# Kernel optimization log

Measured on AMD Instinct MI355X. Metric: run time of the kernel, lower is better.

## Reference

```python
import jax, jax.numpy as jnp
import numpy as np

WIN = 12     # SAMv3 window_size
HEADS = 8    # num_heads

def _window(t, win=WIN):
    B, H, W, C = t.shape
    t = t.reshape(B, H // win, win, W // win, win, C).transpose(0, 1, 3, 2, 4, 5)
    return t.reshape(B, (H // win) * (W // win), win * win, C)

def _unwindow(t, H, W, win=WIN):
    B, nW, S, C = t.shape
    t = t.reshape(B, H // win, W // win, win, win, C).transpose(0, 1, 3, 2, 4, 5)
    return t.reshape(B, H, W, C)

def _sam(fq, fkv, bias, wq, wk, wv, wo, bo):
    # Windowed, masked cross-frame multi-head attention (SAMv3).
    # fq, fkv: (B, C, H, W); bias: (B, nW, 1, 1, S) additive mask bias.
    B, C, H, W = fq.shape
    hd = C // HEADS
    scale = hd ** -0.5
    q = _window(jnp.einsum('bchw,cd->bhwd', fq, wq))   # (B,nW,S,C)
    k = _window(jnp.einsum('bchw,cd->bhwd', fkv, wk))
    v = _window(jnp.einsum('bchw,cd->bhwd', fkv, wv))
    nW, S = q.shape[1], q.shape[2]
    q = q.reshape(B, nW, S, HEADS, hd)
    k = k.reshape(B, nW, S, HEADS, hd)
    v = v.reshape(B, nW, S, HEADS, hd)
    attn = jnp.einsum('bnqhd,bnkhd->bnhqk', q, k) * scale + bias
    attn = jax.nn.softmax(attn, axis=-1)
    out = jnp.einsum('bnhqk,bnkhd->bnqhd', attn, v).reshape(B, nW, S, C)
    out = out @ wo + bo
    return _unwindow(out, H, W).transpose(0, 3, 1, 2)  # (B, C, H, W)

def setup_inputs() -> dict:
    key = jax.random.key(0)
    B, C, T, H, W = 2, 384, 2, 192, 192
    ks = jax.random.split(key, 16)
    d = {}
    d['x'] = jax.random.normal(ks[0], (B, C, T, H, W), jnp.float32)
    d['mask'] = jax.random.randint(ks[1], (B, T, 1, H, W), 0, 2, jnp.int32)
    names = ['sam1_wq', 'sam1_wk', 'sam1_wv', 'sam1_wo',
             'sam2_wq', 'sam2_wk', 'sam2_wv', 'sam2_wo',
             'proj1_w', 'proj2_w']
    for i, n in enumerate(names):
        d[n] = jax.random.normal(ks[2 + i], (C, C), jnp.float32) * 0.02
    d['sam1_bo'] = jnp.zeros((C,), jnp.float32)
    d['sam2_bo'] = jnp.zeros((C,), jnp.float32)
    d['proj1_b'] = jnp.zeros((C,), jnp.float32)
    d['proj2_b'] = jnp.zeros((C,), jnp.float32)
    return d

def reference(x, mask, sam1_wq, sam1_wk, sam1_wv, sam1_wo, sam1_bo,
              sam2_wq, sam2_wk, sam2_wv, sam2_wo, sam2_bo,
              proj1_w, proj1_b, proj2_w, proj2_b):
    # x: (B, C, T=2, H, W); mask: (B, T, 1, H, W)
    f1 = x[:, :, 0]
    f2 = x[:, :, 1]
    m = mask[:, 1, 0][..., None]                      # (B, H, W, 1), frame-2 mask
    mw = _window(m)[..., 0]                           # (B, nW, S)
    bias = jnp.where(mw == 0, -1e9, 0.0).astype(x.dtype)[:, :, None, None, :]
    o1 = _sam(f1, f2, bias, sam1_wq, sam1_wk, sam1_wv, sam1_wo, sam1_bo)
    x1 = jnp.einsum('bchw,dc->bdhw', o1, proj1_w) + proj1_b[None, :, None, None]
    o2 = _sam(f2, f1, bias, sam2_wq, sam2_wk, sam2_wv, sam2_wo, sam2_bo)
    x2 = jnp.einsum('bchw,dc->bdhw', o2, proj2_w) + proj2_b[None, :, None, None]
    return jnp.concatenate([x1[:, :, None], x2[:, :, None]], axis=2)  # (B, C, 2, H, W)
```

## Files before the change

kernel.cpp:

```cpp
#include <hip/hip_runtime.h>
#include <stdint.h>

typedef __attribute__((ext_vector_type(8))) short bf16x8;
typedef __attribute__((ext_vector_type(4))) float f32x4;

#define HW    36864
#define CCH   384
#define NPIX  73728
#define W2    147456

__device__ __forceinline__ unsigned short f2bf(float f) {
  unsigned u = __builtin_bit_cast(unsigned, f);
  u += 0x7FFFu + ((u >> 16) & 1u);
  return (unsigned short)(u >> 16);
}

typedef const unsigned int __attribute__((address_space(1)))* gas1_t;
typedef unsigned int __attribute__((address_space(3)))* las3_t;
__device__ __forceinline__ void gload16(const void* g, void* l) {
  __builtin_amdgcn_global_load_lds((gas1_t)g, (las3_t)l, 16, 0, 0);
}


__global__ void k_wt(const float* __restrict__ w0, const float* __restrict__ w1,
                     const float* __restrict__ w2, const float* __restrict__ w3,
                     const float* __restrict__ w4, const float* __restrict__ w5,
                     unsigned short* __restrict__ wt) {
  int idx = blockIdx.x * 256 + threadIdx.x;
  int w = blockIdx.y;
  const float* W;
  switch (w) { case 0: W = w0; break; case 1: W = w1; break;
               case 2: W = w2; break; case 3: W = w3; break;
               case 4: W = w4; break; default: W = w5; break; }
  int c = idx / 384, d = idx % 384;
  wt[(size_t)w * W2 + (size_t)d * 384 + c] = f2bf(W[(size_t)c * 384 + d]);
}

__global__ void k_wf(const float* __restrict__ wo1, const float* __restrict__ pj1,
                     const float* __restrict__ wo2, const float* __restrict__ pj2,
                     unsigned short* __restrict__ wfT) {
  int idx = blockIdx.x * 256 + threadIdx.x;
  int s = blockIdx.y;
  const float* wo = s ? wo2 : wo1;
  const float* pj = s ? pj2 : pj1;
  int d = idx / 384, e = idx % 384;
  float acc = 0.f;
  for (int c = 0; c < 384; ++c) acc += pj[d * 384 + c] * wo[e * 384 + c];
  wfT[(size_t)s * W2 + (size_t)d * 384 + e] = f2bf(acc);
}

__global__ void k_bf(const float* __restrict__ bo1, const float* __restrict__ pj1,
                     const float* __restrict__ pb1, const float* __restrict__ bo2,
                     const float* __restrict__ pj2, const float* __restrict__ pb2,
                     float* __restrict__ bfused) {
  int t = threadIdx.x;
  int s = t / 384, d = t % 384;
  const float* bo = s ? bo2 : bo1;
  const float* pj = s ? pj2 : pj1;
  const float* pb = s ? pb2 : pb1;
  float acc = pb[d];
  for (int c = 0; c < 384; ++c) acc += pj[d * 384 + c] * bo[c];
  bfused[t] = acc;
}

__global__ __launch_bounds__(256) void k_tx(const float* __restrict__ x,
                                            unsigned short* __restrict__ xbf) {
  __shared__ float tile[64][65];
  int p0 = blockIdx.x * 64;
  int c0 = blockIdx.y * 64;
  int bt = blockIdx.z;
  int b = bt >> 1, t = bt & 1;
  int tid = threadIdx.x;
  int cl = tid >> 2;
  int pq = (tid & 3) * 4;
  const float* src = x + (((size_t)b * CCH + (c0 + cl)) * 2 + t) * HW + p0;
#pragma unroll
  for (int i = 0; i < 4; ++i) {
    int p_l = pq + i * 16;
    float4 v = *reinterpret_cast<const float4*>(src + p_l);
    tile[cl][p_l + 0] = v.x; tile[cl][p_l + 1] = v.y;
    tile[cl][p_l + 2] = v.z; tile[cl][p_l + 3] = v.w;
  }
  __syncthreads();
  int pl = tid >> 2;
  int cq = (tid & 3) * 16;
  unsigned short* dst = xbf + ((size_t)(t * 2 + b) * HW + p0 + pl) * CCH + c0 + cq;
  bf16x8 o0, o1;
#pragma unroll
  for (int j = 0; j < 8; ++j) o0[j] = (short)f2bf(tile[cq + j][pl]);
#pragma unroll
  for (int j = 0; j < 8; ++j) o1[j] = (short)f2bf(tile[cq + 8 + j][pl]);
  *reinterpret_cast<bf16x8*>(dst) = o0;
  *reinterpret_cast<bf16x8*>(dst + 8) = o1;
}

template <int EPI>
__global__ __launch_bounds__(256) void gemm_bt(
    const unsigned short* __restrict__ A,
    const unsigned short* __restrict__ Bt,
    unsigned short* __restrict__ Cb, int ldc,
    float* __restrict__ Cf,
    const float* __restrict__ bias,
    int tsel, float oscale) {
  __shared__ __align__(16) unsigned short Ash[2][4096];
  __shared__ __align__(16) unsigned short Bsh[2][4096];
  const int tid = threadIdx.x;
  const int lane = tid & 63;
  const int wid = tid >> 6, wr = wid >> 1, wc = wid & 1;
  const int m0 = blockIdx.y * 128, n0 = blockIdx.x * 128;
  const int r15 = lane & 15, g = lane >> 4;

  const int u1 = tid + 256;
  const unsigned short* srcA0 = A + (size_t)(m0 + (tid >> 2)) * 384 + (((tid & 3) ^ ((tid >> 3) & 3)) << 3);
  const unsigned short* srcA1 = A + (size_t)(m0 + (u1 >> 2)) * 384 + (((u1 & 3) ^ ((u1 >> 3) & 3)) << 3);
  const unsigned short* srcB0 = Bt + (size_t)(n0 + (tid >> 2)) * 384 + (((tid & 3) ^ ((tid >> 3) & 3)) << 3);
  const unsigned short* srcB1 = Bt + (size_t)(n0 + (u1 >> 2)) * 384 + (((u1 & 3) ^ ((u1 >> 3) & 3)) << 3);
  const int wbase = (tid & ~63) * 8;

  f32x4 acc[4][4];
  f32x4 zero4 = {0.f, 0.f, 0.f, 0.f};
#pragma unroll
  for (int a = 0; a < 4; ++a)
#pragma unroll
    for (int b = 0; b < 4; ++b) acc[a][b] = zero4;

  const int swzr = (g ^ ((r15 >> 1) & 3)) << 3;

#define STAGE(cur, kt) do {                            \
    int ke = (kt) * 32;                                \
    gload16(srcA0 + ke, &Ash[(cur)][wbase]);           \
    gload16(srcA1 + ke, &Ash[(cur)][2048 + wbase]);    \
    gload16(srcB0 + ke, &Bsh[(cur)][wbase]);           \
    gload16(srcB1 + ke, &Bsh[(cur)][2048 + wbase]);    \
  } while (0)

  STAGE(0, 0);
  for (int kt = 0; kt < 12; ++kt) {
    const int cur = kt & 1;
    __syncthreads();
    if (kt < 11) STAGE(cur ^ 1, kt + 1);
    bf16x8 af[4], bfv[4];
#pragma unroll
    for (int a = 0; a < 4; ++a)
      af[a] = *(const bf16x8*)&Ash[cur][(wr * 64 + a * 16 + r15) * 32 + swzr];
#pragma unroll
    for (int b = 0; b < 4; ++b)
      bfv[b] = *(const bf16x8*)&Bsh[cur][(wc * 64 + b * 16 + r15) * 32 + swzr];
#pragma unroll
    for (int a = 0; a < 4; ++a)
#pragma unroll
      for (int b = 0; b < 4; ++b)
        acc[a][b] = __builtin_amdgcn_mfma_f32_16x16x32_bf16(af[a], bfv[b], acc[a][b], 0, 0, 0);
  }
#undef STAGE

  if (EPI == 2) {
    const int bb = m0 / HW;
#pragma unroll
    for (int a = 0; a < 4; ++a) {
#pragma unroll
      for (int r = 0; r < 4; ++r) {
        int m = m0 + wr * 64 + a * 16 + g * 4 + r;
        int p = m - bb * HW;
        int ph = p / 192, pw = p % 192;
        int wy = ph / 12, sy = ph % 12, wx = pw / 12, sx = pw % 12;
        size_t rowoff = ((size_t)bb * HW + (wy * 16 + wx) * 144 + sy * 12 + sx) * (size_t)ldc;
#pragma unroll
        for (int b = 0; b < 4; ++b) {
          int n = n0 + wc * 64 + b * 16 + r15;
          Cb[rowoff + n] = f2bf(acc[a][b][r] * oscale);
        }
      }
    }
  } else {
    int bb = n0 / HW;
#pragma unroll
    for (int a = 0; a < 4; ++a) {
      int d = m0 + wr * 64 + a * 16 + g * 4;
#pragma unroll
      for (int b = 0; b < 4; ++b) {
        int n = n0 + wc * 64 + b * 16 + r15;
        int p = n - bb * HW;
#pragma unroll
        for (int r = 0; r < 4; ++r) {
          float v = acc[a][b][r] + bias[d + r];
          Cf[(((size_t)bb * CCH + (d + r)) * 2 + tsel) * HW + p] = v;
        }
      }
    }
  }
}

__global__ __launch_bounds__(512, 2) void attn_kernel(
    const unsigned short* __restrict__ q,
    const unsigned short* __restrict__ kv,
    const int* __restrict__ mask,
    unsigned short* __restrict__ obuf) {
  __shared__ __align__(16) unsigned short P[8][16][168];
  const int n = blockIdx.x, b = blockIdx.y;
  const int tid = threadIdx.x;
  const int h = tid >> 6, lane = tid & 63;
  const int c15 = lane & 15, g = lane >> 4;
  const int wy = n >> 4, wx = n & 15;
  const unsigned short* qb = q  + ((size_t)b * HW + n * 144) * 384 + h * 48;
  const unsigned short* kb = kv + ((size_t)b * HW + n * 144) * 768 + h * 48;
  const unsigned short* vb = kb + 384;
  const int* mrow = mask + (size_t)(b * 2 + 1) * HW;

  for (int idx = lane; idx < 16 * 24; idx += 64)
    P[h][idx / 24][144 + (idx % 24)] = 0;

  float biasv[9];
#pragma unroll
  for (int nt = 0; nt < 9; ++nt) {
    int sk = nt * 16 + c15;
    int ph = wy * 12 + sk / 12, pw = wx * 12 + sk % 12;
    biasv[nt] = (mrow[ph * 192 + pw] == 0) ? -1e9f : 0.0f;
  }

  bf16x8 zfrag = {0, 0, 0, 0, 0, 0, 0, 0};
  f32x4 zero4 = {0.f, 0.f, 0.f, 0.f};

  bf16x8 kf0[9], kf1[9];
#pragma unroll
  for (int nt = 0; nt < 9; ++nt) {
    const unsigned short* kp = kb + (size_t)(nt * 16 + c15) * 768;
    kf0[nt] = *(const bf16x8*)(kp + g * 8);
    kf1[nt] = zfrag;
    if (g < 2) kf1[nt] = *(const bf16x8*)(kp + 32 + g * 8);
  }

  bf16x8 vf[5][3];
#pragma unroll
  for (int ks = 0; ks < 5; ++ks) {
#pragma unroll
    for (int dt = 0; dt < 3; ++dt) {
      bf16x8 v = {0, 0, 0, 0, 0, 0, 0, 0};
#pragma unroll
      for (int j = 0; j < 8; ++j) {
        int sk = ks * 32 + g * 8 + j;
        if (sk < 144)
          v[j] = (short)vb[(size_t)sk * 768 + dt * 16 + c15];
      }
      vf[ks][dt] = v;
    }
  }

  bf16x8 qf0, qf1;
  {
    const unsigned short* qp = qb + (size_t)c15 * 384;
    qf0 = *(const bf16x8*)(qp + g * 8);
    qf1 = zfrag;
    if (g < 2) qf1 = *(const bf16x8*)(qp + 32 + g * 8);
  }

  for (int mt = 0; mt < 9; ++mt) {
    bf16x8 qn0 = zfrag, qn1 = zfrag;
    if (mt < 8) {
      const unsigned short* qp = qb + (size_t)((mt + 1) * 16 + c15) * 384;
      qn0 = *(const bf16x8*)(qp + g * 8);
      if (g < 2) qn1 = *(const bf16x8*)(qp + 32 + g * 8);
    }

    f32x4 sacc[9];
#pragma unroll
    for (int nt = 0; nt < 9; ++nt) {
      f32x4 t = __builtin_amdgcn_mfma_f32_16x16x32_bf16(qf1, kf1[nt], zero4, 0, 0, 0);
      sacc[nt] = __builtin_amdgcn_mfma_f32_16x16x32_bf16(qf0, kf0[nt], t, 0, 0, 0);
    }

    float l4[4] = {0.f, 0.f, 0.f, 0.f};
#pragma unroll
    for (int nt = 0; nt < 9; ++nt) {
#pragma unroll
      for (int r = 0; r < 4; ++r) {
        float pv = __expf(sacc[nt][r] + biasv[nt]);
        l4[r] += pv;
        P[h][g * 4 + r][nt * 16 + c15] = f2bf(pv);
      }
    }
#pragma unroll
    for (int s = 1; s < 16; s <<= 1)
#pragma unroll
      for (int r = 0; r < 4; ++r) l4[r] += __shfl_xor(l4[r], s, 64);

    f32x4 oacc[3];
#pragma unroll
    for (int dt = 0; dt < 3; ++dt) oacc[dt] = zero4;
#pragma unroll
    for (int ks = 0; ks < 5; ++ks) {
      bf16x8 pf = *(const bf16x8*)&P[h][c15][ks * 32 + g * 8];
#pragma unroll
      for (int dt = 0; dt < 3; ++dt)
        oacc[dt] = __builtin_amdgcn_mfma_f32_16x16x32_bf16(pf, vf[ks][dt], oacc[dt], 0, 0, 0);
    }

    float inv[4];
#pragma unroll
    for (int r = 0; r < 4; ++r) inv[r] = 1.0f / l4[r];
#pragma unroll
    for (int dt = 0; dt < 3; ++dt) {
#pragma unroll
      for (int r = 0; r < 4; ++r) {
        int so = mt * 16 + g * 4 + r;
        int oh = wy * 12 + so / 12, ow = wx * 12 + so % 12;
        obuf[((size_t)b * HW + oh * 192 + ow) * 384 + h * 48 + dt * 16 + c15] =
            f2bf(oacc[dt][r] * inv[r]);
      }
    }

    qf0 = qn0; qf1 = qn1;
  }
}

extern "C" void kernel_launch(void* const* d_in, const int* in_sizes, int n_in,
                              void* d_out, int out_size, void* d_ws, size_t ws_size,
                              hipStream_t stream) {
  const float* x    = (const float*)d_in[0];
  const int*   mask = (const int*)d_in[1];
  const float* wq1 = (const float*)d_in[2];
  const float* wk1 = (const float*)d_in[3];
  const float* wv1 = (const float*)d_in[4];
  const float* wo1 = (const float*)d_in[5];
  const float* wq2 = (const float*)d_in[6];
  const float* wk2 = (const float*)d_in[7];
  const float* wv2 = (const float*)d_in[8];
  const float* wo2 = (const float*)d_in[9];
  const float* pj1 = (const float*)d_in[10];
  const float* pj2 = (const float*)d_in[11];
  const float* bo1 = (const float*)d_in[12];
  const float* bo2 = (const float*)d_in[13];
  const float* pb1 = (const float*)d_in[14];
  const float* pb2 = (const float*)d_in[15];
  float* out = (float*)d_out;

  char* ws = (char*)d_ws;
  size_t off = 0;
  unsigned short* wt   = (unsigned short*)(ws + off); off += (size_t)6 * W2 * 2;
  unsigned short* wfT  = (unsigned short*)(ws + off); off += (size_t)2 * W2 * 2;
  float*          bfu  = (float*)(ws + off);          off += (size_t)2 * 384 * 4;
  unsigned short* xbf  = (unsigned short*)(ws + off); off += (size_t)4 * HW * CCH * 2;
  unsigned short* qbuf = (unsigned short*)(ws + off); off += (size_t)NPIX * 384 * 2;
  unsigned short* kvbuf= (unsigned short*)(ws + off); off += (size_t)NPIX * 768 * 2;
  unsigned short* obuf = (unsigned short*)(ws + off); off += (size_t)NPIX * 384 * 2;
  if (ws_size < off) return;

  k_wt<<<dim3(576, 6), 256, 0, stream>>>(wq1, wk1, wv1, wq2, wk2, wv2, wt);
  k_wf<<<dim3(576, 2), 256, 0, stream>>>(wo1, pj1, wo2, pj2, wfT);
  k_bf<<<1, 768, 0, stream>>>(bo1, pj1, pb1, bo2, pj2, pb2, bfu);
  k_tx<<<dim3(576, 6, 4), 256, 0, stream>>>(x, xbf);

  const float SCALE = 0.14433756729740643f;
  for (int s = 0; s < 2; ++s) {
    const unsigned short* fq = xbf + (size_t)(s == 0 ? 0 : 1) * 2 * HW * CCH;
    const unsigned short* fk = xbf + (size_t)(s == 0 ? 1 : 0) * 2 * HW * CCH;
    gemm_bt<2><<<dim3(3, 576), 256, 0, stream>>>(fq, wt + (size_t)(s * 3 + 0) * W2,
                                                 qbuf, 384, nullptr, nullptr, 0, SCALE);
    gemm_bt<2><<<dim3(6, 576), 256, 0, stream>>>(fk, wt + (size_t)(s * 3 + 1) * W2,
                                                 kvbuf, 768, nullptr, nullptr, 0, 1.0f);
    attn_kernel<<<dim3(256, 2), 512, 0, stream>>>(qbuf, kvbuf, mask, obuf);
    gemm_bt<1><<<dim3(576, 3), 256, 0, stream>>>(wfT + (size_t)s * W2, obuf,
                                                 nullptr, 0, out, bfu + s * 384, s, 1.0f);
  }
}
```

Before: 718.5 us.

## Fuse per-frame Q/KV projections into one GEMM, remap workgroups, interleave attention MMAs

Weights are reordered so that each input frame's Q, K and V projections (Q for one stage, K/V for the other) run as a single 9-column-tile GEMM. This reads each frame's activations once and launches fewer kernels, at the cost of extra workspace for double Q/KV buffers. The GEMM blocks get an XCD-aware workgroup remapping intended to improve L2 locality. The attention kernel now interleaves the PV MFMAs with the QK/exp loop to overlap compute and cut register pressure. A fallback path keeps the old per-stage schedule when workspace is too small.

```diff
diff --git a/kernel.cpp b/kernel.cpp
--- a/kernel.cpp
+++ b/kernel.cpp
@@ -32,8 +32,10 @@
   switch (w) { case 0: W = w0; break; case 1: W = w1; break;
                case 2: W = w2; break; case 3: W = w3; break;
                case 4: W = w4; break; default: W = w5; break; }
+  const int slotmap[6] = {0, 4, 5, 3, 1, 2};
+  int slot = slotmap[w];
   int c = idx / 384, d = idx % 384;
-  wt[(size_t)w * W2 + (size_t)d * 384 + c] = f2bf(W[(size_t)c * 384 + d]);
+  wt[(size_t)slot * W2 + (size_t)d * 384 + c] = f2bf(W[(size_t)c * 384 + d]);
 }
 
 __global__ void k_wf(const float* __restrict__ wo1, const float* __restrict__ pj1,
@@ -98,7 +100,9 @@
 __global__ __launch_bounds__(256) void gemm_bt(
     const unsigned short* __restrict__ A,
     const unsigned short* __restrict__ Bt,
-    unsigned short* __restrict__ Cb, int ldc,
+    unsigned short* __restrict__ Cq,
+    unsigned short* __restrict__ Ckv,
+    int nsplit,
     float* __restrict__ Cf,
     const float* __restrict__ bias,
     int tsel, float oscale) {
@@ -107,7 +111,16 @@
   const int tid = threadIdx.x;
   const int lane = tid & 63;
   const int wid = tid >> 6, wr = wid >> 1, wc = wid & 1;
-  const int m0 = blockIdx.y * 128, n0 = blockIdx.x * 128;
+
+  const int gx = gridDim.x;
+  const int nwg = gx * gridDim.y;
+  const int bid = blockIdx.x + blockIdx.y * gx;
+  const int chunk = nwg >> 3;
+  const int l = (bid & 7) * chunk + (bid >> 3);
+  const int bx = l % gx, by = l / gx;
+
+  const int m0 = (EPI == 1 ? bx : by) * 128;
+  const int n0 = (EPI == 1 ? by : bx) * 128;
   const int r15 = lane & 15, g = lane >> 4;
 
   const int u1 = tid + 256;
@@ -156,6 +169,11 @@
 
   if (EPI == 2) {
     const int bb = m0 / HW;
+    unsigned short* Cp;
+    int ldc, nc0;
+    float sc;
+    if (n0 < nsplit) { Cp = Cq;  ldc = 384; nc0 = n0;          sc = oscale; }
+    else             { Cp = Ckv; ldc = 768; nc0 = n0 - nsplit; sc = 1.0f;   }
 #pragma unroll
     for (int a = 0; a < 4; ++a) {
 #pragma unroll
@@ -167,8 +185,8 @@
         size_t rowoff = ((size_t)bb * HW + (wy * 16 + wx) * 144 + sy * 12 + sx) * (size_t)ldc;
 #pragma unroll
         for (int b = 0; b < 4; ++b) {
-          int n = n0 + wc * 64 + b * 16 + r15;
-          Cb[rowoff + n] = f2bf(acc[a][b][r] * oscale);
+          int n = nc0 + wc * 64 + b * 16 + r15;
+          Cp[rowoff + n] = f2bf(acc[a][b][r] * sc);
         }
       }
     }
@@ -262,38 +280,40 @@
       if (g < 2) qn1 = *(const bf16x8*)(qp + 32 + g * 8);
     }
 
-    f32x4 sacc[9];
+    float l4[4] = {0.f, 0.f, 0.f, 0.f};
+    f32x4 oacc[3];
+#pragma unroll
+    for (int dt = 0; dt < 3; ++dt) oacc[dt] = zero4;
+
 #pragma unroll
     for (int nt = 0; nt < 9; ++nt) {
-      f32x4 t = __builtin_amdgcn_mfma_f32_16x16x32_bf16(qf1, kf1[nt], zero4, 0, 0, 0);
-      sacc[nt] = __builtin_amdgcn_mfma_f32_16x16x32_bf16(qf0, kf0[nt], t, 0, 0, 0);
-    }
-
-    float l4[4] = {0.f, 0.f, 0.f, 0.f};
-#pragma unroll
-    for (int nt = 0; nt < 9; ++nt) {
+      f32x4 s = __builtin_amdgcn_mfma_f32_16x16x32_bf16(qf1, kf1[nt], zero4, 0, 0, 0);
+      s = __builtin_amdgcn_mfma_f32_16x16x32_bf16(qf0, kf0[nt], s, 0, 0, 0);
 #pragma unroll
       for (int r = 0; r < 4; ++r) {
-        float pv = __expf(sacc[nt][r] + biasv[nt]);
+        float pv = __expf(s[r] + biasv[nt]);
         l4[r] += pv;
         P[h][g * 4 + r][nt * 16 + c15] = f2bf(pv);
       }
-    }
+      if (nt & 1) {
+        int ks = nt >> 1;
+        bf16x8 pf = *(const bf16x8*)&P[h][c15][ks * 32 + g * 8];
+#pragma unroll
+        for (int dt = 0; dt < 3; ++dt)
+          oacc[dt] = __builtin_amdgcn_mfma_f32_16x16x32_bf16(pf, vf[ks][dt], oacc[dt], 0, 0, 0);
+      }
+    }
+    {
+      bf16x8 pf = *(const bf16x8*)&P[h][c15][4 * 32 + g * 8];
+#pragma unroll
+      for (int dt = 0; dt < 3; ++dt)
+        oacc[dt] = __builtin_amdgcn_mfma_f32_16x16x32_bf16(pf, vf[4][dt], oacc[dt], 0, 0, 0);
+    }
+
 #pragma unroll
     for (int s = 1; s < 16; s <<= 1)
 #pragma unroll
       for (int r = 0; r < 4; ++r) l4[r] += __shfl_xor(l4[r], s, 64);
-
-    f32x4 oacc[3];
-#pragma unroll
-    for (int dt = 0; dt < 3; ++dt) oacc[dt] = zero4;
-#pragma unroll
-    for (int ks = 0; ks < 5; ++ks) {
-      bf16x8 pf = *(const bf16x8*)&P[h][c15][ks * 32 + g * 8];
-#pragma unroll
-      for (int dt = 0; dt < 3; ++dt)
-        oacc[dt] = __builtin_amdgcn_mfma_f32_16x16x32_bf16(pf, vf[ks][dt], oacc[dt], 0, 0, 0);
-    }
 
     float inv[4];
 #pragma unroll
@@ -334,32 +354,57 @@
   const float* pb2 = (const float*)d_in[15];
   float* out = (float*)d_out;
 
+  const float SCALE = 0.14433756729740643f;
+
   char* ws = (char*)d_ws;
   size_t off = 0;
   unsigned short* wt   = (unsigned short*)(ws + off); off += (size_t)6 * W2 * 2;
   unsigned short* wfT  = (unsigned short*)(ws + off); off += (size_t)2 * W2 * 2;
   float*          bfu  = (float*)(ws + off);          off += (size_t)2 * 384 * 4;
   unsigned short* xbf  = (unsigned short*)(ws + off); off += (size_t)4 * HW * CCH * 2;
-  unsigned short* qbuf = (unsigned short*)(ws + off); off += (size_t)NPIX * 384 * 2;
-  unsigned short* kvbuf= (unsigned short*)(ws + off); off += (size_t)NPIX * 768 * 2;
-  unsigned short* obuf = (unsigned short*)(ws + off); off += (size_t)NPIX * 384 * 2;
-  if (ws_size < off) return;
+  size_t fixed = off;
+
+  size_t qsz = (size_t)NPIX * 384 * 2, kvsz = (size_t)NPIX * 768 * 2, osz = qsz;
+  bool fused = (ws_size >= fixed + 2 * qsz + 2 * kvsz + osz);
+  if (!fused && ws_size < fixed + qsz + kvsz + osz) return;
 
   k_wt<<<dim3(576, 6), 256, 0, stream>>>(wq1, wk1, wv1, wq2, wk2, wv2, wt);
   k_wf<<<dim3(576, 2), 256, 0, stream>>>(wo1, pj1, wo2, pj2, wfT);
   k_bf<<<1, 768, 0, stream>>>(bo1, pj1, pb1, bo2, pj2, pb2, bfu);
   k_tx<<<dim3(576, 6, 4), 256, 0, stream>>>(x, xbf);
 
-  const float SCALE = 0.14433756729740643f;
-  for (int s = 0; s < 2; ++s) {
-    const unsigned short* fq = xbf + (size_t)(s == 0 ? 0 : 1) * 2 * HW * CCH;
-    const unsigned short* fk = xbf + (size_t)(s == 0 ? 1 : 0) * 2 * HW * CCH;
-    gemm_bt<2><<<dim3(3, 576), 256, 0, stream>>>(fq, wt + (size_t)(s * 3 + 0) * W2,
-                                                 qbuf, 384, nullptr, nullptr, 0, SCALE);
-    gemm_bt<2><<<dim3(6, 576), 256, 0, stream>>>(fk, wt + (size_t)(s * 3 + 1) * W2,
-                                                 kvbuf, 768, nullptr, nullptr, 0, 1.0f);
-    attn_kernel<<<dim3(256, 2), 512, 0, stream>>>(qbuf, kvbuf, mask, obuf);
-    gemm_bt<1><<<dim3(576, 3), 256, 0, stream>>>(wfT + (size_t)s * W2, obuf,
-                                                 nullptr, 0, out, bfu + s * 384, s, 1.0f);
-  }
-}
+  if (fused) {
+    unsigned short* qb[2] = {(unsigned short*)(ws + fixed),
+                             (unsigned short*)(ws + fixed + qsz)};
+    unsigned short* kvb[2] = {(unsigned short*)(ws + fixed + 2 * qsz),
+                              (unsigned short*)(ws + fixed + 2 * qsz + kvsz)};
+    unsigned short* obuf = (unsigned short*)(ws + fixed + 2 * qsz + 2 * kvsz);
+    for (int f = 0; f < 2; ++f) {
+      gemm_bt<2><<<dim3(9, 576), 256, 0, stream>>>(
+          xbf + (size_t)f * 2 * HW * CCH, wt + (size_t)f * 3 * W2,
+          qb[f], kvb[1 - f], 384, nullptr, nullptr, 0, SCALE);
+    }
+    for (int s = 0; s < 2; ++s) {
+      attn_kernel<<<dim3(256, 2), 512, 0, stream>>>(qb[s], kvb[s], mask, obuf);
+      gemm_bt<1><<<dim3(3, 576), 256, 0, stream>>>(
+          wfT + (size_t)s * W2, obuf, nullptr, nullptr, 0, out, bfu + s * 384, s, 1.0f);
+    }
+  } else {
+    unsigned short* qbuf = (unsigned short*)(ws + fixed);
+    unsigned short* kvbuf = (unsigned short*)(ws + fixed + qsz);
+    unsigned short* obuf = (unsigned short*)(ws + fixed + qsz + kvsz);
+    for (int s = 0; s < 2; ++s) {
+      const unsigned short* fq = xbf + (size_t)(s == 0 ? 0 : 1) * 2 * HW * CCH;
+      const unsigned short* fk = xbf + (size_t)(s == 0 ? 1 : 0) * 2 * HW * CCH;
+      gemm_bt<2><<<dim3(3, 576), 256, 0, stream>>>(
+          fq, wt + (size_t)(s == 0 ? 0 : 3) * W2, qbuf, nullptr, 384,
+          nullptr, nullptr, 0, SCALE);
+      gemm_bt<2><<<dim3(6, 576), 256, 0, stream>>>(
+          fk, wt + (size_t)(s == 0 ? 4 : 1) * W2, nullptr, kvbuf, 0,
+          nullptr, nullptr, 0, 1.0f);
+      attn_kernel<<<dim3(256, 2), 512, 0, stream>>>(qbuf, kvbuf, mask, obuf);
+      gemm_bt<1><<<dim3(3, 576), 256, 0, stream>>>(
+          wfT + (size_t)s * W2, obuf, nullptr, nullptr, 0, out, bfu + s * 384, s, 1.0f);
+    }
+  }
+}
```

Result: no change. 723.6 us (+0.7%).
